# Optimization experiments

Measured on AMD Instinct MI355X. Metric: run time of the kernel, lower is better.

## Reference

```python
import jax, jax.numpy as jnp
import numpy as np

E, D, H, F = 1024, 64, 16, 4096  # embedding, per-head dim, heads, mlp hidden
B, S = 2, 2048
EPS = 1e-5


def _layernorm(x, g, b):
    m = jnp.mean(x, axis=-1, keepdims=True)
    v = jnp.mean((x - m) ** 2, axis=-1, keepdims=True)
    return (x - m) * jax.lax.rsqrt(v + EPS) * g + b


def setup_inputs() -> dict:
    key = jax.random.key(0)
    ks = jax.random.split(key, 12)
    s_e = 1.0 / np.sqrt(E)
    s_f = 1.0 / np.sqrt(F)
    return {
        "x": jax.random.normal(ks[0], (B, S, E), jnp.float32),
        "Wq": jax.random.normal(ks[1], (H, E, D), jnp.float32) * s_e,
        "bq": jnp.zeros((H, D), jnp.float32),
        "Wk": jax.random.normal(ks[2], (H, E, D), jnp.float32) * s_e,
        "bk": jnp.zeros((H, D), jnp.float32),
        "Wv": jax.random.normal(ks[3], (H, E, D), jnp.float32) * s_e,
        "bv": jnp.zeros((H, D), jnp.float32),
        "Wo": jax.random.normal(ks[4], (E, E), jnp.float32) * s_e,
        "bo": jnp.zeros((E,), jnp.float32),
        "ln1_g": jnp.ones((E,), jnp.float32),
        "ln1_b": jnp.zeros((E,), jnp.float32),
        "ln2_g": jnp.ones((E,), jnp.float32),
        "ln2_b": jnp.zeros((E,), jnp.float32),
        "W1": jax.random.normal(ks[5], (E, F), jnp.float32) * s_e,
        "b1": jnp.zeros((F,), jnp.float32),
        "W2": jax.random.normal(ks[6], (F, E), jnp.float32) * s_f,
        "b2": jnp.zeros((E,), jnp.float32),
    }


def reference(x, Wq, bq, Wk, bk, Wv, bv, Wo, bo, ln1_g, ln1_b, ln2_g, ln2_b, W1, b1, W2, b2):
    h = _layernorm(x, ln1_g, ln1_b)
    # batched-head projections: [H,B,S,D]
    q = jnp.einsum("bse,hed->hbsd", h, Wq) + bq[:, None, None, :]
    k = jnp.einsum("bse,hed->hbsd", h, Wk) + bk[:, None, None, :]
    v = jnp.einsum("bse,hed->hbsd", h, Wv) + bv[:, None, None, :]
    # faithful quirk: scores = K @ Q^T (no 1/sqrt(d)), softmax over query axis
    scores = jnp.einsum("hbsd,hbtd->hbst", k, q)  # [H,B,S_key,S_query]
    att = jax.nn.softmax(scores, axis=-1)
    o = jnp.einsum("hbst,hbtd->hbsd", att, v)  # [H,B,S,D]
    o = jnp.transpose(o, (1, 2, 0, 3)).reshape(x.shape[0], x.shape[1], -1)  # concat heads
    x = x + o @ Wo + bo
    m = _layernorm(x, ln2_g, ln2_b)
    m = jax.nn.relu(m @ W1 + b1) @ W2 + b2
    return x + m
```

## Files before the change

### kernel.cpp

```cpp
#include <hip/hip_runtime.h>
#include <cstdint>
#include <cstddef>

typedef __attribute__((ext_vector_type(8))) short short8;
typedef __attribute__((ext_vector_type(4))) float f32x4;
typedef __attribute__((ext_vector_type(4))) unsigned short ushort4v;

#define E_DIM 1024
#define D_DIM 64
#define H_DIM 16
#define F_DIM 4096
#define B_DIM 2
#define S_DIM 2048
#define M_DIM 4096
#define LN_EPS 1e-5f
#define LOG2E 1.4426950408889634f

__device__ __forceinline__ float bf2f(unsigned short u) {
  union { unsigned int i; float f; } v;
  v.i = ((unsigned int)u) << 16;
  return v.f;
}
__device__ __forceinline__ unsigned short f2bf(float f) {
  union { float f; unsigned int i; } v;
  v.f = f;
  unsigned int r = v.i + 0x7FFFu + ((v.i >> 16) & 1u);
  return (unsigned short)(r >> 16);
}
__device__ __forceinline__ unsigned int cvt_pk_bf16(float a, float b) {
  unsigned int r;
  asm("v_cvt_pk_bf16_f32 %0, %1, %2" : "=v"(r) : "v"(a), "v"(b));
  return r;
}
__device__ __forceinline__ float exp2_fast(float x) {
  float r;
  asm("v_exp_f32 %0, %1" : "=v"(r) : "v"(x));
  return r;
}

__device__ __forceinline__ void gload_lds16(const unsigned short* src,
                                            unsigned short* dst) {
  __builtin_amdgcn_global_load_lds(
      (const __attribute__((address_space(1))) void*)src,
      (__attribute__((address_space(3))) void*)dst, 16, 0, 0);
}

template <bool QKV>
__global__ __launch_bounds__(256) void transpose_w(
    const float* __restrict__ in, unsigned short* __restrict__ ohi, int R,
    int C, float scale) {
  __shared__ float t[32][33];
  const int c0 = blockIdx.x * 32, r0 = blockIdx.y * 32;
  const int tid = threadIdx.x;
  {
    const int rr = tid >> 3, c4 = (tid & 7) * 4;
    size_t addr;
    if (QKV)
      addr = (size_t)(c0 >> 6) * 65536 + (size_t)(r0 + rr) * 64 +
             ((c0 & 63) + c4);
    else
      addr = (size_t)(r0 + rr) * C + (c0 + c4);
    float4 v = *(const float4*)(in + addr);
    t[rr][c4 + 0] = v.x;
    t[rr][c4 + 1] = v.y;
    t[rr][c4 + 2] = v.z;
    t[rr][c4 + 3] = v.w;
  }
  __syncthreads();
  {
    const int cc = tid >> 3, k4 = (tid & 7) * 4;
    ushort4v hi;
    hi.x = f2bf(t[k4 + 0][cc] * scale);
    hi.y = f2bf(t[k4 + 1][cc] * scale);
    hi.z = f2bf(t[k4 + 2][cc] * scale);
    hi.w = f2bf(t[k4 + 3][cc] * scale);
    *(ushort4v*)(ohi + (size_t)(c0 + cc) * R + (r0 + k4)) = hi;
  }
}

__global__ __launch_bounds__(256) void ln_kernel(const float* __restrict__ x,
                                                 const float* __restrict__ g,
                                                 const float* __restrict__ b,
                                                 unsigned short* __restrict__ o) {
  const int row = blockIdx.x;
  const float* xp = x + (size_t)row * E_DIM;
  const int t4 = threadIdx.x * 4;
  float4 xv = *(const float4*)(xp + t4);
  float s = xv.x + xv.y + xv.z + xv.w;
  float ss = xv.x * xv.x + xv.y * xv.y + xv.z * xv.z + xv.w * xv.w;
#pragma unroll
  for (int off = 32; off > 0; off >>= 1) {
    s += __shfl_down(s, off);
    ss += __shfl_down(ss, off);
  }
  __shared__ float red[8];
  const int wid = threadIdx.x >> 6;
  if ((threadIdx.x & 63) == 0) {
    red[wid] = s;
    red[4 + wid] = ss;
  }
  __syncthreads();
  if (threadIdx.x == 0) {
    float S = red[0] + red[1] + red[2] + red[3];
    float SS = red[4] + red[5] + red[6] + red[7];
    float mean = S * (1.0f / E_DIM);
    float var = SS * (1.0f / E_DIM) - mean * mean;
    red[0] = mean;
    red[1] = rsqrtf(var + LN_EPS);
  }
  __syncthreads();
  const float mean = red[0], rstd = red[1];
  float4 gv = *(const float4*)(g + t4);
  float4 bv = *(const float4*)(b + t4);
  ushort4v hi;
  hi.x = f2bf((xv.x - mean) * rstd * gv.x + bv.x);
  hi.y = f2bf((xv.y - mean) * rstd * gv.y + bv.y);
  hi.z = f2bf((xv.z - mean) * rstd * gv.z + bv.z);
  hi.w = f2bf((xv.w - mean) * rstd * gv.w + bv.w);
  *(ushort4v*)(o + (size_t)row * E_DIM + t4) = hi;
}

template <int MODE>
__global__ __launch_bounds__(256) void mfma_gemm(
    const unsigned short* __restrict__ A, const unsigned short* __restrict__ B,
    const float* __restrict__ bias, const float* __restrict__ bias2,
    const float* __restrict__ bias3, void* __restrict__ out0,
    void* __restrict__ out1, void* __restrict__ out2, int M, int N, int K) {
  __shared__ unsigned short As[8192];
  __shared__ unsigned short Bs[8192];
  const int tid = threadIdx.x;
  const int m0 = blockIdx.y * 128, n0 = blockIdx.x * 128;
  const int lane = tid & 63, wid = tid >> 6;
  const int wr = wid >> 1, wc = wid & 1;
  const int lr = lane & 15, lg = lane >> 4;

  f32x4 acc[4][4];
#pragma unroll
  for (int i = 0; i < 4; ++i)
#pragma unroll
    for (int j = 0; j < 4; ++j) acc[i][j] = {0.f, 0.f, 0.f, 0.f};

  int kbeg = 0, kend = K;
  if constexpr (MODE == 4) {
    int kslice = K / gridDim.z;
    kbeg = blockIdx.z * kslice;
    kend = kbeg + kslice;
  }

  for (int k0 = kbeg; k0 < kend; k0 += 64) {
#pragma unroll
    for (int c = 0; c < 4; ++c) {
      int chunk = wid * 4 + c;
      int rb = chunk >> 1, kc = chunk & 1;
      size_t goff = (size_t)(rb * 16 + lr) * K + k0 + kc * 32 + lg * 8;
      gload_lds16(A + (size_t)m0 * K + goff, As + chunk * 512);
      gload_lds16(B + (size_t)n0 * K + goff, Bs + chunk * 512);
    }
    __syncthreads();
#pragma unroll
    for (int kc = 0; kc < 2; ++kc) {
      short8 af[4], bf[4];
#pragma unroll
      for (int mi = 0; mi < 4; ++mi)
        af[mi] = *(const short8*)(As + ((wr * 4 + mi) * 2 + kc) * 512 + lane * 8);
#pragma unroll
      for (int ni = 0; ni < 4; ++ni)
        bf[ni] = *(const short8*)(Bs + ((wc * 4 + ni) * 2 + kc) * 512 + lane * 8);
      __builtin_amdgcn_s_setprio(1);
#pragma unroll
      for (int mi = 0; mi < 4; ++mi)
#pragma unroll
        for (int ni = 0; ni < 4; ++ni)
          acc[mi][ni] = __builtin_amdgcn_mfma_f32_16x16x32_bf16(
              af[mi], bf[ni], acc[mi][ni], 0, 0, 0);
      __builtin_amdgcn_s_setprio(0);
    }
    __syncthreads();
  }
#pragma unroll
  for (int mi = 0; mi < 4; ++mi) {
#pragma unroll
    for (int ni = 0; ni < 4; ++ni) {
      int n = n0 + wc * 64 + ni * 16 + lr;
#pragma unroll
      for (int rr = 0; rr < 4; ++rr) {
        int m = m0 + wr * 64 + mi * 16 + lg * 4 + rr;
        float v = acc[mi][ni][rr];
        if constexpr (MODE == 0) {
          int seg = n >> 10, nn = n & 1023;
          const float* bp = seg == 0 ? bias : seg == 1 ? bias2 : bias3;
          v += (seg == 0) ? bp[nn] * LOG2E : bp[nn];
          int hh = nn >> 6, d = nn & 63, bb = m >> 11, srow = m & 2047;
          size_t pb = (size_t)(hh * 2 + bb) * 131072;
          if (seg == 0)
            ((unsigned short*)out0)[pb + (size_t)srow * 64 + d] = f2bf(v);
          else if (seg == 1)
            ((unsigned short*)out1)[pb + (size_t)srow * 64 + d] = f2bf(v);
          else
            ((unsigned short*)out2)[pb + (size_t)d * 2048 + srow] = f2bf(v);
        } else if constexpr (MODE == 3) {
          ((unsigned short*)out0)[(size_t)m * N + n] = f2bf(fmaxf(v + bias[n], 0.f));
        } else {
          unsafeAtomicAdd((float*)out0 + (size_t)m * N + n, v);
        }
      }
    }
  }
}

__global__ __launch_bounds__(256, 4) void attn_mfma(
    const unsigned short* __restrict__ Q, const unsigned short* __restrict__ K,
    const unsigned short* __restrict__ Vt, unsigned short* __restrict__ O) {
  __shared__ unsigned short Qs[2][4096];
  __shared__ unsigned short Vs[2][4096];
  const int bid = blockIdx.x;
  const int wg = (bid & 7) * 128 + (bid >> 3);
  const int pair = wg >> 5, stile = wg & 31;
  const int tid = threadIdx.x, lane = tid & 63, wid = tid >> 6;
  const int lr = lane & 15, lg = lane >> 4;
  const size_t pbase = (size_t)pair * 131072;

  const int s_own = stile * 64 + wid * 16 + lr;
  short8 kb[2];
#pragma unroll
  for (int c = 0; c < 2; ++c)
    kb[c] = *(const short8*)(K + pbase + (size_t)s_own * 64 + c * 32 + lg * 8);

  f32x4 oa[4];
#pragma unroll
  for (int i = 0; i < 4; ++i) oa[i] = {0.f, 0.f, 0.f, 0.f};
  float mrun = -3e38f, lrun = 0.f;

  auto stage = [&](int buf, int t0) {
#pragma unroll
    for (int c = 0; c < 2; ++c) {
      int chunk = wid * 2 + c;
      gload_lds16(Q + pbase + (size_t)(t0 + wid * 16 + lr) * 64 + c * 32 + lg * 8,
                  &Qs[buf][chunk * 512]);
      gload_lds16(Vt + pbase + (size_t)(wid * 16 + lr) * 2048 + t0 + c * 32 + lg * 8,
                  &Vs[buf][chunk * 512]);
    }
  };

  stage(0, 0);
  __syncthreads();

  for (int it = 0; it < 32; ++it) {
    const int cur = it & 1;
    if (it < 31) stage(cur ^ 1, (it + 1) * 64);

    f32x4 sacc[4];
#pragma unroll
    for (int j = 0; j < 4; ++j) {
      sacc[j] = {0.f, 0.f, 0.f, 0.f};
      __builtin_amdgcn_s_setprio(1);
#pragma unroll
      for (int c = 0; c < 2; ++c) {
        short8 aq = *(const short8*)(&Qs[cur][(j * 2 + c) * 512 + lane * 8]);
        sacc[j] = __builtin_amdgcn_mfma_f32_16x16x32_bf16(aq, kb[c], sacc[j], 0, 0, 0);
      }
      __builtin_amdgcn_s_setprio(0);
    }
    float tm = fmaxf(
        fmaxf(fmaxf(fmaxf(sacc[0][0], sacc[0][1]), fmaxf(sacc[0][2], sacc[0][3])),
              fmaxf(fmaxf(sacc[1][0], sacc[1][1]), fmaxf(sacc[1][2], sacc[1][3]))),
        fmaxf(fmaxf(fmaxf(sacc[2][0], sacc[2][1]), fmaxf(sacc[2][2], sacc[2][3])),
              fmaxf(fmaxf(sacc[3][0], sacc[3][1]), fmaxf(sacc[3][2], sacc[3][3]))));
    tm = fmaxf(tm, __shfl_xor(tm, 16));
    tm = fmaxf(tm, __shfl_xor(tm, 32));
    if (!__all(tm - mrun <= 11.0f)) {
      float mnew = fmaxf(mrun, tm);
      float sc = exp2_fast(mrun - mnew);
      mrun = mnew;
      lrun *= sc;
#pragma unroll
      for (int di = 0; di < 4; ++di) {
        f32x4 t = oa[di];
        t[0] *= sc; t[1] *= sc; t[2] *= sc; t[3] *= sc;
        oa[di] = t;
      }
    }
    float p[4][4];
#pragma unroll
    for (int j = 0; j < 4; ++j)
#pragma unroll
      for (int r = 0; r < 4; ++r) p[j][r] = exp2_fast(sacc[j][r] - mrun);
    float lsum = ((p[0][0] + p[0][1]) + (p[0][2] + p[0][3])) +
                 ((p[1][0] + p[1][1]) + (p[1][2] + p[1][3])) +
                 ((p[2][0] + p[2][1]) + (p[2][2] + p[2][3])) +
                 ((p[3][0] + p[3][1]) + (p[3][2] + p[3][3]));
    lsum += __shfl_xor(lsum, 16);
    lsum += __shfl_xor(lsum, 32);
    lrun += lsum;
    unsigned int pw[4][2];
#pragma unroll
    for (int j = 0; j < 4; ++j) {
      pw[j][0] = cvt_pk_bf16(p[j][0], p[j][1]);
      pw[j][1] = cvt_pk_bf16(p[j][2], p[j][3]);
    }
#pragma unroll
    for (int kc = 0; kc < 2; ++kc) {
      unsigned int bw[4];
#pragma unroll
      for (int mm = 0; mm < 4; ++mm) {
        int src = ((lg & 1) * 2 + (mm >> 1)) * 16 + lr;
        int lo = __shfl((int)pw[2 * kc][mm & 1], src, 64);
        int hi = __shfl((int)pw[2 * kc + 1][mm & 1], src, 64);
        bw[mm] = (lg & 2) ? (unsigned)hi : (unsigned)lo;
      }
      union { unsigned int u[4]; short8 s8; } pb;
      pb.u[0] = bw[0]; pb.u[1] = bw[1]; pb.u[2] = bw[2]; pb.u[3] = bw[3];
      __builtin_amdgcn_s_setprio(1);
#pragma unroll
      for (int di = 0; di < 4; ++di) {
        short8 vf = *(const short8*)(&Vs[cur][(di * 2 + kc) * 512 + lane * 8]);
        oa[di] = __builtin_amdgcn_mfma_f32_16x16x32_bf16(vf, pb.s8, oa[di], 0, 0, 0);
      }
      __builtin_amdgcn_s_setprio(0);
    }
    __syncthreads();
  }

  const float inv = 1.f / lrun;
  const int b = pair & 1, h = pair >> 1;
  unsigned short* op = O + ((size_t)(b * 2048 + s_own)) * 1024 + h * 64;
#pragma unroll
  for (int di = 0; di < 4; ++di) {
    unsigned int w0 = cvt_pk_bf16(oa[di][0] * inv, oa[di][1] * inv);
    unsigned int w1 = cvt_pk_bf16(oa[di][2] * inv, oa[di][3] * inv);
    *(unsigned int*)(op + di * 16 + lg * 4) = w0;
    *(unsigned int*)(op + di * 16 + lg * 4 + 2) = w1;
  }
}

__global__ __launch_bounds__(256) void init_acc(const float* __restrict__ resid,
                                                const float* __restrict__ bias,
                                                float* __restrict__ out) {
  int i = blockIdx.x * 256 + threadIdx.x;
  float4 v = ((const float4*)resid)[i];
  float4 bb = ((const float4*)bias)[i & 255];
  v.x += bb.x; v.y += bb.y; v.z += bb.z; v.w += bb.w;
  ((float4*)out)[i] = v;
}

extern "C" void kernel_launch(void* const* d_in, const int* in_sizes, int n_in,
                              void* d_out, int out_size, void* d_ws,
                              size_t ws_size, hipStream_t stream) {
  const float* x = (const float*)d_in[0];
  const float* Wq = (const float*)d_in[1];
  const float* bq = (const float*)d_in[2];
  const float* Wk = (const float*)d_in[3];
  const float* bk = (const float*)d_in[4];
  const float* Wv = (const float*)d_in[5];
  const float* bv = (const float*)d_in[6];
  const float* Wo = (const float*)d_in[7];
  const float* bo = (const float*)d_in[8];
  const float* ln1_g = (const float*)d_in[9];
  const float* ln1_b = (const float*)d_in[10];
  const float* ln2_g = (const float*)d_in[11];
  const float* ln2_b = (const float*)d_in[12];
  const float* W1 = (const float*)d_in[13];
  const float* b1 = (const float*)d_in[14];
  const float* W2 = (const float*)d_in[15];
  const float* b2 = (const float*)d_in[16];

  char* w = (char*)d_ws;
  const size_t MB = 1024 * 1024;
  unsigned short* WqkvT = (unsigned short*)(w + 0 * MB);
  unsigned short* WoT = (unsigned short*)(w + 6 * MB);
  unsigned short* W1T = (unsigned short*)(w + 8 * MB);
  unsigned short* W2T = (unsigned short*)(w + 16 * MB);
  unsigned short* h = (unsigned short*)(w + 24 * MB);
  unsigned short* Qb = (unsigned short*)(w + 32 * MB);
  unsigned short* Kb = (unsigned short*)(w + 40 * MB);
  unsigned short* Vt = (unsigned short*)(w + 48 * MB);
  unsigned short* Obuf = (unsigned short*)(w + 56 * MB);
  unsigned short* m1 = (unsigned short*)(w + 32 * MB);
  float* x2 = (float*)(w + 64 * MB);

  const dim3 blk(256);

  transpose_w<true><<<dim3(32, 32), blk, 0, stream>>>(Wq, WqkvT, 1024, 1024, LOG2E);
  transpose_w<true><<<dim3(32, 32), blk, 0, stream>>>(Wk, WqkvT + 1048576, 1024, 1024, 1.f);
  transpose_w<true><<<dim3(32, 32), blk, 0, stream>>>(Wv, WqkvT + 2097152, 1024, 1024, 1.f);
  transpose_w<false><<<dim3(32, 32), blk, 0, stream>>>(Wo, WoT, 1024, 1024, 1.f);
  transpose_w<false><<<dim3(128, 32), blk, 0, stream>>>(W1, W1T, 1024, 4096, 1.f);
  transpose_w<false><<<dim3(32, 128), blk, 0, stream>>>(W2, W2T, 4096, 1024, 1.f);

  ln_kernel<<<M_DIM, blk, 0, stream>>>(x, ln1_g, ln1_b, h);

  mfma_gemm<0><<<dim3(24, 32), blk, 0, stream>>>(h, WqkvT, bq, bk, bv, Qb, Kb,
                                                 Vt, M_DIM, 3072, 1024);

  attn_mfma<<<1024, blk, 0, stream>>>(Qb, Kb, Vt, Obuf);

  init_acc<<<4096, blk, 0, stream>>>(x, bo, x2);
  mfma_gemm<4><<<dim3(8, 32, 2), blk, 0, stream>>>(Obuf, WoT, nullptr, nullptr,
                                                   nullptr, x2, nullptr,
                                                   nullptr, M_DIM, 1024, 1024);

  ln_kernel<<<M_DIM, blk, 0, stream>>>(x2, ln2_g, ln2_b, h);

  mfma_gemm<3><<<dim3(32, 32), blk, 0, stream>>>(h, W1T, b1, nullptr, nullptr,
                                                 m1, nullptr, nullptr, M_DIM,
                                                 4096, 1024);

  init_acc<<<4096, blk, 0, stream>>>(x2, b2, (float*)d_out);
  mfma_gemm<4><<<dim3(8, 32, 2), blk, 0, stream>>>(
      m1, W2T, nullptr, nullptr, nullptr, (float*)d_out, nullptr, nullptr,
      M_DIM, 1024, 4096);
}
```

Measured before the change: 494.2 us.

## Fuse weight transposes, swizzle GEMM tiles, drop setprio, deepen W2 split-K

Merges the six weight-transpose launches into a single kernel that picks its source matrix from the block index, cutting launch overhead. The GEMM remaps workgroup IDs with a stride-8 swizzle, which may change L2 reuse across the chiplets. It also removes the s_setprio around the MFMA loop and raises the W2 split-K factor from 2 to 4 for more parallelism. The cost is more atomic accumulation traffic into the output and possibly weaker scheduling without the priority hints.

```diff
diff --git a/kernel.cpp b/kernel.cpp
--- a/kernel.cpp
+++ b/kernel.cpp
@@ -45,17 +45,40 @@
       (__attribute__((address_space(3))) void*)dst, 16, 0, 0);
 }
 
-template <bool QKV>
-__global__ __launch_bounds__(256) void transpose_w(
-    const float* __restrict__ in, unsigned short* __restrict__ ohi, int R,
-    int C, float scale) {
+__global__ __launch_bounds__(256) void transpose_all(
+    const float* __restrict__ Wq, const float* __restrict__ Wk,
+    const float* __restrict__ Wv, const float* __restrict__ Wo,
+    const float* __restrict__ W1, const float* __restrict__ W2,
+    unsigned short* __restrict__ WqkvT, unsigned short* __restrict__ WoT,
+    unsigned short* __restrict__ W1T, unsigned short* __restrict__ W2T) {
+  int id = blockIdx.x;
+  const float* in;
+  unsigned short* out;
+  int R, C;
+  bool qkv = false;
+  float scale = 1.f;
+  if (id < 3072) {
+    int seg = id >> 10;
+    in = seg == 0 ? Wq : seg == 1 ? Wk : Wv;
+    out = WqkvT + (size_t)seg * 1048576;
+    R = 1024; C = 1024; qkv = true;
+    if (seg == 0) scale = LOG2E;
+    id &= 1023;
+  } else if (id < 4096) {
+    in = Wo; out = WoT; R = 1024; C = 1024; id -= 3072;
+  } else if (id < 8192) {
+    in = W1; out = W1T; R = 1024; C = 4096; id -= 4096;
+  } else {
+    in = W2; out = W2T; R = 4096; C = 1024; id -= 8192;
+  }
+  const int tpc = C >> 5;
+  const int c0 = (id % tpc) * 32, r0 = (id / tpc) * 32;
   __shared__ float t[32][33];
-  const int c0 = blockIdx.x * 32, r0 = blockIdx.y * 32;
   const int tid = threadIdx.x;
   {
     const int rr = tid >> 3, c4 = (tid & 7) * 4;
     size_t addr;
-    if (QKV)
+    if (qkv)
       addr = (size_t)(c0 >> 6) * 65536 + (size_t)(r0 + rr) * 64 +
              ((c0 & 63) + c4);
     else
@@ -74,7 +97,7 @@
     hi.y = f2bf(t[k4 + 1][cc] * scale);
     hi.z = f2bf(t[k4 + 2][cc] * scale);
     hi.w = f2bf(t[k4 + 3][cc] * scale);
-    *(ushort4v*)(ohi + (size_t)(c0 + cc) * R + (r0 + k4)) = hi;
+    *(ushort4v*)(out + (size_t)(c0 + cc) * R + (r0 + k4)) = hi;
   }
 }
 
@@ -129,7 +152,10 @@
   __shared__ unsigned short As[8192];
   __shared__ unsigned short Bs[8192];
   const int tid = threadIdx.x;
-  const int m0 = blockIdx.y * 128, n0 = blockIdx.x * 128;
+  const int nwg = gridDim.x * gridDim.y;
+  const int flat = blockIdx.y * gridDim.x + blockIdx.x;
+  const int swz = (flat & 7) * (nwg >> 3) + (flat >> 3);
+  const int m0 = (swz / gridDim.x) * 128, n0 = (swz % gridDim.x) * 128;
   const int lane = tid & 63, wid = tid >> 6;
   const int wr = wid >> 1, wc = wid & 1;
   const int lr = lane & 15, lg = lane >> 4;
@@ -166,14 +192,12 @@
 #pragma unroll
       for (int ni = 0; ni < 4; ++ni)
         bf[ni] = *(const short8*)(Bs + ((wc * 4 + ni) * 2 + kc) * 512 + lane * 8);
-      __builtin_amdgcn_s_setprio(1);
 #pragma unroll
       for (int mi = 0; mi < 4; ++mi)
 #pragma unroll
         for (int ni = 0; ni < 4; ++ni)
           acc[mi][ni] = __builtin_amdgcn_mfma_f32_16x16x32_bf16(
               af[mi], bf[ni], acc[mi][ni], 0, 0, 0);
-      __builtin_amdgcn_s_setprio(0);
     }
     __syncthreads();
   }
@@ -380,12 +404,8 @@
 
   const dim3 blk(256);
 
-  transpose_w<true><<<dim3(32, 32), blk, 0, stream>>>(Wq, WqkvT, 1024, 1024, LOG2E);
-  transpose_w<true><<<dim3(32, 32), blk, 0, stream>>>(Wk, WqkvT + 1048576, 1024, 1024, 1.f);
-  transpose_w<true><<<dim3(32, 32), blk, 0, stream>>>(Wv, WqkvT + 2097152, 1024, 1024, 1.f);
-  transpose_w<false><<<dim3(32, 32), blk, 0, stream>>>(Wo, WoT, 1024, 1024, 1.f);
-  transpose_w<false><<<dim3(128, 32), blk, 0, stream>>>(W1, W1T, 1024, 4096, 1.f);
-  transpose_w<false><<<dim3(32, 128), blk, 0, stream>>>(W2, W2T, 4096, 1024, 1.f);
+  transpose_all<<<12288, blk, 0, stream>>>(Wq, Wk, Wv, Wo, W1, W2, WqkvT, WoT,
+                                           W1T, W2T);
 
   ln_kernel<<<M_DIM, blk, 0, stream>>>(x, ln1_g, ln1_b, h);
 
@@ -406,7 +426,7 @@
                                                  4096, 1024);
 
   init_acc<<<4096, blk, 0, stream>>>(x2, b2, (float*)d_out);
-  mfma_gemm<4><<<dim3(8, 32, 2), blk, 0, stream>>>(
+  mfma_gemm<4><<<dim3(8, 32, 4), blk, 0, stream>>>(
       m1, W2T, nullptr, nullptr, nullptr, (float*)d_out, nullptr, nullptr,
       M_DIM, 1024, 4096);
 }
```

New measurement: 515.1 us. 1.04x slower.
